# Kernel optimization log

Hardware: AMD Instinct MI355X
Metric: run time of the kernel (lower is better)

The kernel has to match this reference:

```python
import jax, jax.numpy as jnp
import numpy as np

N_NODES = 100_000
N_EDGES = 800_000
N_RELS = 2
NEG_SLOPE = 0.2  # DGL GATConv default negative_slope


def _gat_conv(x, src, dst, W, al, ar, b, n_nodes):
    """One DGL-style GATConv over one relation's edge list.
    x: (N, F_in); src/dst: (E,); W: (F_in, H*D); al/ar: (H, D); b: (H*D,).
    Returns (N, H, D). Zero in-degree nodes get just the bias (softmax empty)."""
    H, D = al.shape
    feat = (x @ W).reshape(-1, H, D)                      # (N, H, D)
    el = jnp.sum(feat * al, axis=-1)                      # (N, H)
    er = jnp.sum(feat * ar, axis=-1)                      # (N, H)
    e = jax.nn.leaky_relu(el[src] + er[dst], NEG_SLOPE)   # (E, H) edge scores
    # segment softmax over incoming edges of each dst node
    m = jax.ops.segment_max(e, dst, num_segments=n_nodes)  # (N, H)
    m = jax.lax.stop_gradient(jnp.where(jnp.isfinite(m), m, 0.0))
    ex = jnp.exp(e - m[dst])                              # (E, H)
    s = jax.ops.segment_sum(ex, dst, num_segments=n_nodes)  # (N, H)
    alpha = ex / s[dst]                                   # (E, H); s[dst] > 0 on edges
    # weighted scatter-aggregate of source features
    out = jax.ops.segment_sum(alpha[:, :, None] * feat[src], dst,
                              num_segments=n_nodes)       # (N, H, D)
    return out + b.reshape(H, D)


def reference(x, W1, al1, ar1, b1, W2, al2, ar2, b2, src, dst):
    n = x.shape[0]
    n_rels = src.shape[0]
    # layer 1: per-relation GATConv (2 heads), mean across relations
    h1 = sum(_gat_conv(x, src[r], dst[r], W1[r], al1[r], ar1[r], b1[r], n)
             for r in range(n_rels)) / n_rels             # (N, 2, 64)
    h1 = jax.nn.relu(h1.reshape(n, -1))                   # flatten(1) + relu -> (N, 128)
    # layer 2: per-relation GATConv (1 head), mean across relations, squeeze head
    h2 = sum(_gat_conv(h1, src[r], dst[r], W2[r], al2[r], ar2[r], b2[r], n)
             for r in range(n_rels)) / n_rels             # (N, 1, 128)
    return h2[:, 0, :]                                    # (N, 128)


def setup_inputs() -> dict:
    key = jax.random.key(0)
    ks = jax.random.split(key, 11)
    f = lambda k, s: jax.random.normal(k, s, dtype=jnp.float32) * 0.1
    return {
        "x": jax.random.normal(ks[0], (N_NODES, 128), dtype=jnp.float32),
        "W1": f(ks[1], (N_RELS, 128, 128)),
        "al1": f(ks[2], (N_RELS, 2, 64)),
        "ar1": f(ks[3], (N_RELS, 2, 64)),
        "b1": jnp.zeros((N_RELS, 128), jnp.float32),
        "W2": f(ks[4], (N_RELS, 128, 128)),
        "al2": f(ks[5], (N_RELS, 1, 128)),
        "ar2": f(ks[6], (N_RELS, 1, 128)),
        "b2": jnp.zeros((N_RELS, 128), jnp.float32),
        "src": jax.random.randint(ks[7], (N_RELS, N_EDGES), 0, N_NODES, dtype=jnp.int32),
        "dst": jax.random.randint(ks[8], (N_RELS, N_EDGES), 0, N_NODES, dtype=jnp.int32),
    }
```

## Files before the change

### kernel.cpp

```cpp
#include <hip/hip_runtime.h>
#include <hip/hip_bf16.h>
#include <math.h>

#define NN 100000
#define NE 800000
#define FD 128

#define BKW 512
#define NBK 391
#define CAP 4608
#define CHUNK 8192

typedef unsigned short ushort_t;
typedef __attribute__((ext_vector_type(8))) short bf16x8;
typedef __attribute__((ext_vector_type(4))) float f32x4;

union U8 { uint4 u; bf16x8 b; };

__device__ inline unsigned f2bf(float f){
    unsigned u = __float_as_uint(f);
    return (u + 0x7fffu + ((u >> 16) & 1u)) >> 16;
}
__device__ inline unsigned cvtpk(float lo, float hi){
    unsigned r;
    asm("v_cvt_pk_bf16_f32 %0, %1, %2" : "=v"(r) : "v"(lo), "v"(hi));
    return r;
}
__device__ inline float blo(unsigned p){ return __uint_as_float(p << 16); }
__device__ inline float bhi(unsigned p){ return __uint_as_float(p & 0xffff0000u); }
__device__ inline float2 up2(unsigned p){ float2 f; f.x = blo(p); f.y = bhi(p); return f; }
__device__ inline void pkfma(float2& d, float2 a, float2 b){
    asm("v_pk_fma_f32 %0, %1, %2, %0" : "+v"(d) : "v"(a), "v"(b));
}

__global__ __launch_bounds__(256) void k_part(const int* __restrict__ dst,
                                              const int* __restrict__ src,
                                              int* __restrict__ bcur,
                                              uint2* __restrict__ ebuf){
    __shared__ int lcount[NBK];
    __shared__ int lbase[NBK];
    int t = threadIdx.x;
    long base = (long)blockIdx.x * CHUNK;
    for (int j = t; j < NBK; j += 256) lcount[j] = 0;
    __syncthreads();
    #pragma unroll 4
    for (int k = 0; k < CHUNK/256; k++){
        long i = base + k*256 + t;
        if (i < 2*NE){
            int b = (dst[i] + ((i >= NE) ? NN : 0)) >> 9;
            atomicAdd(&lcount[b], 1);
        }
    }
    __syncthreads();
    for (int j = t; j < NBK; j += 256){
        int c = lcount[j];
        lbase[j] = c ? atomicAdd(&bcur[j], c) : 0;
    }
    __syncthreads();
    for (int j = t; j < NBK; j += 256) lcount[j] = 0;
    __syncthreads();
    #pragma unroll 4
    for (int k = 0; k < CHUNK/256; k++){
        long i = base + k*256 + t;
        if (i < 2*NE){
            int dstU = dst[i] + ((i >= NE) ? NN : 0);
            int b = dstU >> 9;
            int r = atomicAdd(&lcount[b], 1);
            int pos = lbase[b] + r;
            if (pos < (b + 1) * CAP)
                ebuf[pos] = make_uint2((unsigned)src[i], (unsigned)dstU);
        }
    }
}

__global__ __launch_bounds__(512) void k_bktscan(const int* __restrict__ bcur,
                                                 int* __restrict__ gbase,
                                                 int* __restrict__ rowptr){
    __shared__ int sm[512];
    int t = threadIdx.x;
    int v = (t < NBK) ? min(bcur[t] - t*CAP, CAP) : 0;
    sm[t] = v; __syncthreads();
    for (int off = 1; off < 512; off <<= 1){
        int add = (t >= off) ? sm[t-off] : 0;
        __syncthreads();
        sm[t] += add;
        __syncthreads();
    }
    if (t <= NBK) gbase[t] = sm[t] - v;
    if (t == 0) rowptr[2*NN] = 2*NE;
}

__global__ __launch_bounds__(256) void k_bscatter(const uint2* __restrict__ ebuf,
                                                  const int* __restrict__ bcur,
                                                  const int* __restrict__ gbase,
                                                  int* __restrict__ rowptr,
                                                  int* __restrict__ colsrc){
    __shared__ uint2 se[CAP];
    __shared__ int lhist[BKW];
    __shared__ int lcur[BKW];
    __shared__ int sm[256];
    int b = blockIdx.x;
    int n0 = b * BKW;
    int nloc = min(2*NN, n0 + BKW) - n0;
    int ecnt = min(bcur[b] - b*CAP, CAP);
    const uint2* eb = ebuf + (size_t)b * CAP;
    int t = threadIdx.x;
    lhist[2*t] = 0; lhist[2*t+1] = 0;
    __syncthreads();
    for (int i = t; i < ecnt; i += 256){
        uint2 e = eb[i];
        se[i] = e;
        atomicAdd(&lhist[e.y - n0], 1);
    }
    __syncthreads();
    int a0 = lhist[2*t], a1 = lhist[2*t+1];
    int ps = a0 + a1;
    sm[t] = ps; __syncthreads();
    for (int off = 1; off < 256; off <<= 1){
        int add = (t >= off) ? sm[t-off] : 0;
        __syncthreads();
        sm[t] += add;
        __syncthreads();
    }
    int excl = sm[t] - ps;
    int g = gbase[b];
    int p0 = g + excl, p1 = g + excl + a0;
    if (2*t     < nloc) rowptr[n0 + 2*t]     = p0;
    if (2*t + 1 < nloc) rowptr[n0 + 2*t + 1] = p1;
    lcur[2*t] = p0; lcur[2*t+1] = p1;
    __syncthreads();
    for (int i = t; i < ecnt; i += 256){
        uint2 e = se[i];
        int p = atomicAdd(&lcur[e.y - n0], 1);
        colsrc[p] = (int)e.x;
    }
}

__global__ void k_prepw2(const float* __restrict__ W1, const float* __restrict__ W2,
                         ushort_t* __restrict__ Wt1, ushort_t* __restrict__ Wt2,
                         int* __restrict__ bcur){
    int idx = blockIdx.x * blockDim.x + threadIdx.x;
    if (idx >= 65536){
        int t = idx - 65536;
        if (t < NBK) bcur[t] = t * CAP;
        return;
    }
    int m = idx >> 15;
    int i = idx & 32767;
    const float* W = m ? W2 : W1;
    ushort_t* Wt   = m ? Wt2 : Wt1;
    int j  = i & 7;
    int l  = (i >> 3) & 63;
    int ks = (i >> 9) & 3;
    int f  = i >> 11;
    int k  = ks*32 + (l >> 4)*8 + j;
    if (m) k = (((k & 7) >> 1) + 4*(k & 1))*16 + (k >> 3);
    int col = (f & 7)*16 + (l & 15);
    int rel = f >> 3;
    Wt[i] = (ushort_t)f2bf(W[rel*16384 + k*FD + col]);
}

__device__ inline float red16(float v){
    v += __shfl_xor(v, 1);
    v += __shfl_xor(v, 2);
    v += __shfl_xor(v, 4);
    v += __shfl_xor(v, 8);
    return v;
}

template<int H, bool AF32>
__global__ __launch_bounds__(256) void k_gemm_mfma(
        const ushort_t* __restrict__ Ab, const float* __restrict__ Af,
        const ushort_t* __restrict__ Wt,
        const float* __restrict__ al0, const float* __restrict__ ar0,
        const float* __restrict__ al1, const float* __restrict__ ar1,
        ushort_t* __restrict__ featb0, ushort_t* __restrict__ featb1,
        float* __restrict__ el0, float* __restrict__ er0,
        float* __restrict__ el1, float* __restrict__ er1){
    int t = threadIdx.x;
    int w = t >> 6, l = t & 63;
    int c = l & 15, kgrp = l >> 4;
    const bf16x8* WtV = (const bf16x8*)Wt;
    long arow = (long)blockIdx.x*64 + w*16 + c;
    bf16x8 zero8 = {0,0,0,0,0,0,0,0};
    bf16x8 af[4];
    bool rok = arow < NN;
    if (AF32){
        const float4* xv = (const float4*)Af;
        #pragma unroll
        for (int ks = 0; ks < 4; ks++){
            if (rok){
                float4 u = xv[arow*32 + (ks*4 + kgrp)*2];
                float4 v = xv[arow*32 + (ks*4 + kgrp)*2 + 1];
                U8 q;
                q.u = make_uint4(cvtpk(u.x,u.y), cvtpk(u.z,u.w),
                                 cvtpk(v.x,v.y), cvtpk(v.z,v.w));
                af[ks] = q.b;
            } else af[ks] = zero8;
        }
    } else {
        const bf16x8* AbV = (const bf16x8*)Ab;
        #pragma unroll
        for (int ks = 0; ks < 4; ks++)
            af[ks] = rok ? AbV[arow*16 + ks*4 + kgrp] : zero8;
    }
    f32x4 acc[16];
    #pragma unroll
    for (int f = 0; f < 16; f++) acc[f] = (f32x4){0.f,0.f,0.f,0.f};
    #pragma unroll
    for (int f = 0; f < 16; f++){
        #pragma unroll
        for (int ks = 0; ks < 4; ks++){
            acc[f] = __builtin_amdgcn_mfma_f32_16x16x32_bf16(
                         af[ks], WtV[(f*4 + ks)*64 + l], acc[f], 0, 0, 0);
        }
    }
    float alv0[8], arv0[8], alv1[8], arv1[8];
    #pragma unroll
    for (int f = 0; f < 8; f++){
        alv0[f] = al0[f*16 + c]; arv0[f] = ar0[f*16 + c];
        alv1[f] = al1[f*16 + c]; arv1[f] = ar1[f*16 + c];
    }
    #pragma unroll
    for (int reg = 0; reg < 4; reg++){
        long orow = (long)blockIdx.x*64 + w*16 + kgrp*4 + reg;
        bool ok = orow < NN;
        if (ok){
            uint4 p0, p1;
            p0.x = cvtpk(acc[0][reg],  acc[4][reg]);
            p0.y = cvtpk(acc[1][reg],  acc[5][reg]);
            p0.z = cvtpk(acc[2][reg],  acc[6][reg]);
            p0.w = cvtpk(acc[3][reg],  acc[7][reg]);
            p1.x = cvtpk(acc[8][reg],  acc[12][reg]);
            p1.y = cvtpk(acc[9][reg],  acc[13][reg]);
            p1.z = cvtpk(acc[10][reg], acc[14][reg]);
            p1.w = cvtpk(acc[11][reg], acc[15][reg]);
            *(uint4*)&featb0[orow*FD + c*8] = p0;
            *(uint4*)&featb1[orow*FD + c*8] = p1;
        }
        if (H == 2){
            float pl00=0, pr00=0, pl01=0, pr01=0;
            float pl10=0, pr10=0, pl11=0, pr11=0;
            #pragma unroll
            for (int f = 0; f < 4; f++){
                pl00 = fmaf(acc[f][reg],    alv0[f],   pl00);
                pr00 = fmaf(acc[f][reg],    arv0[f],   pr00);
                pl01 = fmaf(acc[4+f][reg],  alv0[4+f], pl01);
                pr01 = fmaf(acc[4+f][reg],  arv0[4+f], pr01);
                pl10 = fmaf(acc[8+f][reg],  alv1[f],   pl10);
                pr10 = fmaf(acc[8+f][reg],  arv1[f],   pr10);
                pl11 = fmaf(acc[12+f][reg], alv1[4+f], pl11);
                pr11 = fmaf(acc[12+f][reg], arv1[4+f], pr11);
            }
            pl00 = red16(pl00); pr00 = red16(pr00);
            pl01 = red16(pl01); pr01 = red16(pr01);
            pl10 = red16(pl10); pr10 = red16(pr10);
            pl11 = red16(pl11); pr11 = red16(pr11);
            if (c == 0 && ok){
                el0[orow*2] = pl00; el0[orow*2+1] = pl01;
                er0[orow*2] = pr00; er0[orow*2+1] = pr01;
                el1[orow*2] = pl10; el1[orow*2+1] = pl11;
                er1[orow*2] = pr10; er1[orow*2+1] = pr11;
            }
        } else {
            float pl0=0, pr0=0, pl1=0, pr1=0;
            #pragma unroll
            for (int f = 0; f < 8; f++){
                pl0 = fmaf(acc[f][reg],   alv0[f], pl0);
                pr0 = fmaf(acc[f][reg],   arv0[f], pr0);
                pl1 = fmaf(acc[8+f][reg], alv1[f], pl1);
                pr1 = fmaf(acc[8+f][reg], arv1[f], pr1);
            }
            pl0 = red16(pl0); pr0 = red16(pr0);
            pl1 = red16(pl1); pr1 = red16(pr1);
            if (c == 0 && ok){
                el0[orow] = pl0; er0[orow] = pr0;
                el1[orow] = pl1; er1[orow] = pr1;
            }
        }
    }
}

template<int H>
__global__ __launch_bounds__(256) void k_agg2(
                       const int* __restrict__ rowptr,
                       const int* __restrict__ colsrc,
                       const float* __restrict__ el0, const float* __restrict__ er0,
                       const float* __restrict__ el1, const float* __restrict__ er1,
                       const ushort_t* __restrict__ featb0, const ushort_t* __restrict__ featb1,
                       const float* __restrict__ bias0, const float* __restrict__ bias1,
                       ushort_t* __restrict__ outb, float* __restrict__ outf){
    __shared__ float4 stg[4][2][2][32];
    int wid  = threadIdx.x >> 6;
    int lane = threadIdx.x & 63;
    int half = lane >> 5;
    int hl   = lane & 31;
    int sub  = lane & 15;
    int g    = (lane >> 4) & 1;
    int node = ((blockIdx.x * blockDim.x + threadIdx.x) >> 6) * 2 + half;
    if (node >= NN) return;
    int base0 = rowptr[node],       end0 = rowptr[node+1];
    int base1 = rowptr[NN + node],  end1 = rowptr[NN + node + 1];
    bool has0 = end0 > base0, has1 = end1 > base1;
    float er00 = er0[node*H];
    float er01 = (H == 2) ? er0[node*H + 1] : 0.f;
    float er10 = er1[node*H];
    float er11 = (H == 2) ? er1[node*H + 1] : 0.f;
    float2 ap0[4], ap1[4];
    #pragma unroll
    for (int i = 0; i < 4; i++){ ap0[i] = make_float2(0.f,0.f); ap1[i] = make_float2(0.f,0.f); }
    float s00=0.f, s01=0.f, s10=0.f, s11=0.f;
    while (base0 < end0 || base1 < end1){
        int nrem0 = end0 - base0, nrem1 = end1 - base1;
        bool act0 = hl < nrem0, act1 = hl < nrem1;
        int sv0 = act0 ? colsrc[base0 + hl] : 0;
        int sv1 = act1 ? colsrc[base1 + hl] : 0;
        float a00=0.f, a01=0.f, a10=0.f, a11=0.f;
        if (act0){
            if (H == 2){
                float2 e2 = *(const float2*)&el0[sv0*2];
                float e0 = e2.x + er00, e1 = e2.y + er01;
                e0 = (e0 > 0.f) ? e0 : 0.2f*e0;
                e1 = (e1 > 0.f) ? e1 : 0.2f*e1;
                a00 = __expf(e0); a01 = __expf(e1);
            } else {
                float e0 = el0[sv0] + er00;
                e0 = (e0 > 0.f) ? e0 : 0.2f*e0;
                a00 = __expf(e0);
            }
        }
        if (act1){
            if (H == 2){
                float2 e2 = *(const float2*)&el1[sv1*2];
                float e0 = e2.x + er10, e1 = e2.y + er11;
                e0 = (e0 > 0.f) ? e0 : 0.2f*e0;
                e1 = (e1 > 0.f) ? e1 : 0.2f*e1;
                a10 = __expf(e0); a11 = __expf(e1);
            } else {
                float e0 = el1[sv1] + er10;
                e0 = (e0 > 0.f) ? e0 : 0.2f*e0;
                a10 = __expf(e0);
            }
        }
        s00 += a00; s01 += a01; s10 += a10; s11 += a11;
        stg[wid][half][0][hl] = make_float4(__int_as_float(sv0), a00,
                                            (H == 2) ? a01 : a00, 0.f);
        stg[wid][half][1][hl] = make_float4(__int_as_float(sv1), a10,
                                            (H == 2) ? a11 : a10, 0.f);
        __builtin_amdgcn_sched_barrier(0);
        int nn0 = (nrem0 > 0) ? min(32, nrem0) : 0;
        int nn1 = (nrem1 > 0) ? min(32, nrem1) : 0;
        int nnm = (nn0 > nn1) ? nn0 : nn1;
        for (int j4 = 0; j4 < nnm; j4 += 4){
            int sA = j4 + g, sB = sA + 2;
            float4 e0A = stg[wid][half][0][sA];
            float4 e0B = stg[wid][half][0][sB];
            float4 e1A = stg[wid][half][1][sA];
            float4 e1B = stg[wid][half][1][sB];
            uint4 p0A = *(const uint4*)&featb0[__float_as_uint(e0A.x)*FD + sub*8];
            uint4 p0B = *(const uint4*)&featb0[__float_as_uint(e0B.x)*FD + sub*8];
            uint4 p1A = *(const uint4*)&featb1[__float_as_uint(e1A.x)*FD + sub*8];
            uint4 p1B = *(const uint4*)&featb1[__float_as_uint(e1B.x)*FD + sub*8];
            float2 w0A = make_float2(e0A.y, e0A.z);
            float2 w0B = make_float2(e0B.y, e0B.z);
            float2 w1A = make_float2(e1A.y, e1A.z);
            float2 w1B = make_float2(e1B.y, e1B.z);
            pkfma(ap0[0], w0A, up2(p0A.x));
            pkfma(ap0[1], w0A, up2(p0A.y));
            pkfma(ap0[2], w0A, up2(p0A.z));
            pkfma(ap0[3], w0A, up2(p0A.w));
            pkfma(ap0[0], w0B, up2(p0B.x));
            pkfma(ap0[1], w0B, up2(p0B.y));
            pkfma(ap0[2], w0B, up2(p0B.z));
            pkfma(ap0[3], w0B, up2(p0B.w));
            pkfma(ap1[0], w1A, up2(p1A.x));
            pkfma(ap1[1], w1A, up2(p1A.y));
            pkfma(ap1[2], w1A, up2(p1A.z));
            pkfma(ap1[3], w1A, up2(p1A.w));
            pkfma(ap1[0], w1B, up2(p1B.x));
            pkfma(ap1[1], w1B, up2(p1B.y));
            pkfma(ap1[2], w1B, up2(p1B.z));
            pkfma(ap1[3], w1B, up2(p1B.w));
        }
        base0 += 32; base1 += 32;
    }
    #pragma unroll
    for (int off = 16; off > 0; off >>= 1){
        s00 += __shfl_xor(s00, off);
        s10 += __shfl_xor(s10, off);
        if (H == 2){ s01 += __shfl_xor(s01, off); s11 += __shfl_xor(s11, off); }
    }
    #pragma unroll
    for (int i = 0; i < 4; i++){
        ap0[i].x += __shfl_xor(ap0[i].x, 16); ap0[i].y += __shfl_xor(ap0[i].y, 16);
        ap1[i].x += __shfl_xor(ap1[i].x, 16); ap1[i].y += __shfl_xor(ap1[i].y, 16);
    }
    if (hl < 16){
        float i00 = has0 ? 1.f/s00 : 0.f;
        float i01 = (H == 2) ? (has0 ? 1.f/s01 : 0.f) : i00;
        float i10 = has1 ? 1.f/s10 : 0.f;
        float i11 = (H == 2) ? (has1 ? 1.f/s11 : 0.f) : i10;
        float2 vp[4];
        #pragma unroll
        for (int t = 0; t < 4; t++){
            float bx = bias0[t*16 + sub]       + bias1[t*16 + sub];
            float by = bias0[(t+4)*16 + sub]   + bias1[(t+4)*16 + sub];
            vp[t].x = 0.5f*(ap0[t].x*i00 + ap1[t].x*i10 + bx);
            vp[t].y = 0.5f*(ap0[t].y*i01 + ap1[t].y*i11 + by);
        }
        if (H == 2){
            #pragma unroll
            for (int t = 0; t < 4; t++){
                vp[t].x = fmaxf(vp[t].x, 0.f);
                vp[t].y = fmaxf(vp[t].y, 0.f);
            }
            uint4 o;
            o.x = cvtpk(vp[0].x, vp[0].y); o.y = cvtpk(vp[1].x, vp[1].y);
            o.z = cvtpk(vp[2].x, vp[2].y); o.w = cvtpk(vp[3].x, vp[3].y);
            *(uint4*)&outb[(size_t)node*FD + sub*8] = o;
        } else {
            #pragma unroll
            for (int t = 0; t < 4; t++){
                outf[(size_t)node*FD + t*16 + sub]     = vp[t].x;
                outf[(size_t)node*FD + (t+4)*16 + sub] = vp[t].y;
            }
        }
    }
}

extern "C" void kernel_launch(void* const* d_in, const int* in_sizes, int n_in,
                              void* d_out, int out_size, void* d_ws, size_t ws_size,
                              hipStream_t stream){
    const float* x   = (const float*)d_in[0];
    const float* W1  = (const float*)d_in[1];
    const float* al1 = (const float*)d_in[2];
    const float* ar1 = (const float*)d_in[3];
    const float* b1  = (const float*)d_in[4];
    const float* W2  = (const float*)d_in[5];
    const float* al2 = (const float*)d_in[6];
    const float* ar2 = (const float*)d_in[7];
    const float* b2  = (const float*)d_in[8];
    const int*   src = (const int*)d_in[9];
    const int*   dst = (const int*)d_in[10];
    float* out = (float*)d_out;

    size_t off = 0;
    auto carve = [&](size_t bytes) -> char* {
        char* p = (char*)d_ws + off;
        off += (bytes + 255) & ~(size_t)255;
        return p;
    };
    ushort_t* h1b    = (ushort_t*)carve((size_t)NN * FD * 2);
    ushort_t* featb0 = (ushort_t*)carve((size_t)NN * FD * 2);
    ushort_t* featb1 = (ushort_t*)carve((size_t)NN * FD * 2);
    ushort_t* Wt1    = (ushort_t*)carve(32768 * 2);
    ushort_t* Wt2    = (ushort_t*)carve(32768 * 2);
    float* el0      = (float*)carve((size_t)NN * 2 * 4);
    float* er0      = (float*)carve((size_t)NN * 2 * 4);
    float* el1      = (float*)carve((size_t)NN * 2 * 4);
    float* er1      = (float*)carve((size_t)NN * 2 * 4);
    int*   rowptrA  = (int*)  carve((size_t)(2*NN + 1) * 4);
    int*   colsrcA  = (int*)  carve((size_t)2*NE * 4);
    int*   bcur     = (int*)  carve((size_t)NBK * 4);
    int*   gbase    = (int*)  carve((size_t)(NBK + 1) * 4);
    if (off > ws_size) return;
    uint2* ebuf = (uint2*)featb0;

    const int PB = (2*NE + CHUNK - 1) / CHUNK;
    const int GB = (NN + 63) / 64;
    const int WB = (NN + 7) / 8;
    const int PWB = (65536 + NBK + 255) / 256;

    k_prepw2<<<PWB, 256, 0, stream>>>(W1, W2, Wt1, Wt2, bcur);

    k_part<<<PB, 256, 0, stream>>>(dst, src, bcur, ebuf);
    k_bktscan<<<1, 512, 0, stream>>>(bcur, gbase, rowptrA);
    k_bscatter<<<NBK, 256, 0, stream>>>(ebuf, bcur, gbase, rowptrA, colsrcA);

    k_gemm_mfma<2, true><<<GB, 256, 0, stream>>>(nullptr, x, Wt1,
                                           al1, ar1, al1 + FD, ar1 + FD,
                                           featb0, featb1, el0, er0, el1, er1);
    k_agg2<2><<<WB, 256, 0, stream>>>(rowptrA, colsrcA,
                                      el0, er0, el1, er1, featb0, featb1,
                                      b1, b1 + FD, h1b, nullptr);

    k_gemm_mfma<1, false><<<GB, 256, 0, stream>>>(h1b, nullptr, Wt2,
                                           al2, ar2, al2 + FD, ar2 + FD,
                                           featb0, featb1, el0, er0, el1, er1);
    k_agg2<1><<<WB, 256, 0, stream>>>(rowptrA, colsrcA,
                                      el0, er0, el1, er1, featb0, featb1,
                                      b2, b2 + FD, nullptr, out);
}
```

Measured before the change: 283.9 us.

## Merge CSR build and layer-1 GEMM into fewer launches with atomic bucket bases

Packs the edge partition and the weight conversion into one launch, and the bucket scatter and the first-layer GEMM into a second launch, so independent work runs side by side. The global bucket scan kernel is removed. Each bucket block now claims its output base with an atomic counter, and rows are described by separate begin/end arrays instead of a single rowptr. ebuf gets its own workspace buffer so it no longer aliases featb0, which the concurrent GEMM writes. Buckets are laid out out of order in colsrc, and a memset launch is added to reset the counters.

After: 260.8 us. 8.1% less time.

```diff
diff --git a/kernel.cpp b/kernel.cpp
--- a/kernel.cpp
+++ b/kernel.cpp
@@ -10,6 +10,8 @@
 #define NBK 391
 #define CAP 4608
 #define CHUNK 8192
+#define PB   196
+#define GB   1563
 
 typedef unsigned short ushort_t;
 typedef __attribute__((ext_vector_type(8))) short bf16x8;
@@ -33,10 +35,9 @@
     asm("v_pk_fma_f32 %0, %1, %2, %0" : "+v"(d) : "v"(a), "v"(b));
 }
 
-__global__ __launch_bounds__(256) void k_part(const int* __restrict__ dst,
-                                              const int* __restrict__ src,
-                                              int* __restrict__ bcur,
-                                              uint2* __restrict__ ebuf){
+
+__device__ void part_body(const int* __restrict__ dst, const int* __restrict__ src,
+                          int* __restrict__ bcur, uint2* __restrict__ ebuf){
     __shared__ int lcount[NBK];
     __shared__ int lbase[NBK];
     int t = threadIdx.x;
@@ -67,84 +68,15 @@
             int b = dstU >> 9;
             int r = atomicAdd(&lcount[b], 1);
             int pos = lbase[b] + r;
-            if (pos < (b + 1) * CAP)
-                ebuf[pos] = make_uint2((unsigned)src[i], (unsigned)dstU);
-        }
-    }
-}
-
-__global__ __launch_bounds__(512) void k_bktscan(const int* __restrict__ bcur,
-                                                 int* __restrict__ gbase,
-                                                 int* __restrict__ rowptr){
-    __shared__ int sm[512];
-    int t = threadIdx.x;
-    int v = (t < NBK) ? min(bcur[t] - t*CAP, CAP) : 0;
-    sm[t] = v; __syncthreads();
-    for (int off = 1; off < 512; off <<= 1){
-        int add = (t >= off) ? sm[t-off] : 0;
-        __syncthreads();
-        sm[t] += add;
-        __syncthreads();
-    }
-    if (t <= NBK) gbase[t] = sm[t] - v;
-    if (t == 0) rowptr[2*NN] = 2*NE;
-}
-
-__global__ __launch_bounds__(256) void k_bscatter(const uint2* __restrict__ ebuf,
-                                                  const int* __restrict__ bcur,
-                                                  const int* __restrict__ gbase,
-                                                  int* __restrict__ rowptr,
-                                                  int* __restrict__ colsrc){
-    __shared__ uint2 se[CAP];
-    __shared__ int lhist[BKW];
-    __shared__ int lcur[BKW];
-    __shared__ int sm[256];
-    int b = blockIdx.x;
-    int n0 = b * BKW;
-    int nloc = min(2*NN, n0 + BKW) - n0;
-    int ecnt = min(bcur[b] - b*CAP, CAP);
-    const uint2* eb = ebuf + (size_t)b * CAP;
-    int t = threadIdx.x;
-    lhist[2*t] = 0; lhist[2*t+1] = 0;
-    __syncthreads();
-    for (int i = t; i < ecnt; i += 256){
-        uint2 e = eb[i];
-        se[i] = e;
-        atomicAdd(&lhist[e.y - n0], 1);
-    }
-    __syncthreads();
-    int a0 = lhist[2*t], a1 = lhist[2*t+1];
-    int ps = a0 + a1;
-    sm[t] = ps; __syncthreads();
-    for (int off = 1; off < 256; off <<= 1){
-        int add = (t >= off) ? sm[t-off] : 0;
-        __syncthreads();
-        sm[t] += add;
-        __syncthreads();
-    }
-    int excl = sm[t] - ps;
-    int g = gbase[b];
-    int p0 = g + excl, p1 = g + excl + a0;
-    if (2*t     < nloc) rowptr[n0 + 2*t]     = p0;
-    if (2*t + 1 < nloc) rowptr[n0 + 2*t + 1] = p1;
-    lcur[2*t] = p0; lcur[2*t+1] = p1;
-    __syncthreads();
-    for (int i = t; i < ecnt; i += 256){
-        uint2 e = se[i];
-        int p = atomicAdd(&lcur[e.y - n0], 1);
-        colsrc[p] = (int)e.x;
-    }
-}
-
-__global__ void k_prepw2(const float* __restrict__ W1, const float* __restrict__ W2,
-                         ushort_t* __restrict__ Wt1, ushort_t* __restrict__ Wt2,
-                         int* __restrict__ bcur){
-    int idx = blockIdx.x * blockDim.x + threadIdx.x;
-    if (idx >= 65536){
-        int t = idx - 65536;
-        if (t < NBK) bcur[t] = t * CAP;
-        return;
-    }
+            if (pos < CAP)
+                ebuf[(size_t)b*CAP + pos] = make_uint2((unsigned)src[i], (unsigned)dstU);
+        }
+    }
+}
+
+__device__ void prepw_body(int idx, const float* __restrict__ W1,
+                           const float* __restrict__ W2,
+                           ushort_t* __restrict__ Wt1, ushort_t* __restrict__ Wt2){
     int m = idx >> 15;
     int i = idx & 32767;
     const float* W = m ? W2 : W1;
@@ -160,6 +92,48 @@
     Wt[i] = (ushort_t)f2bf(W[rel*16384 + k*FD + col]);
 }
 
+__device__ void bscatter_body(int b, const uint2* __restrict__ ebuf,
+                              const int* __restrict__ bcur, int* __restrict__ gcounter,
+                              int* __restrict__ rowbeg, int* __restrict__ rowend,
+                              int* __restrict__ colsrc){
+    __shared__ int lhist[BKW];
+    __shared__ int lcur[BKW];
+    __shared__ int sm[256];
+    __shared__ int gb;
+    int n0 = b * BKW;
+    int nloc = min(2*NN, n0 + BKW) - n0;
+    int ecnt = min(bcur[b], CAP);
+    const uint2* eb = ebuf + (size_t)b * CAP;
+    int t = threadIdx.x;
+    lhist[2*t] = 0; lhist[2*t+1] = 0;
+    __syncthreads();
+    for (int i = t; i < ecnt; i += 256)
+        atomicAdd(&lhist[eb[i].y - n0], 1);
+    __syncthreads();
+    int a0 = lhist[2*t], a1 = lhist[2*t+1];
+    int ps = a0 + a1;
+    sm[t] = ps; __syncthreads();
+    for (int off = 1; off < 256; off <<= 1){
+        int add = (t >= off) ? sm[t-off] : 0;
+        __syncthreads();
+        sm[t] += add;
+        __syncthreads();
+    }
+    if (t == 255) gb = atomicAdd(gcounter, sm[255]);
+    __syncthreads();
+    int excl = sm[t] - ps;
+    int p0 = gb + excl, p1 = gb + excl + a0;
+    if (2*t < nloc){ rowbeg[n0 + 2*t] = p0; rowend[n0 + 2*t] = p0 + a0; }
+    if (2*t + 1 < nloc){ rowbeg[n0 + 2*t + 1] = p1; rowend[n0 + 2*t + 1] = p1 + a1; }
+    lcur[2*t] = p0; lcur[2*t+1] = p1;
+    __syncthreads();
+    for (int i = t; i < ecnt; i += 256){
+        uint2 e = eb[i];
+        int p = atomicAdd(&lcur[e.y - n0], 1);
+        colsrc[p] = (int)e.x;
+    }
+}
+
 __device__ inline float red16(float v){
     v += __shfl_xor(v, 1);
     v += __shfl_xor(v, 2);
@@ -169,7 +143,7 @@
 }
 
 template<int H, bool AF32>
-__global__ __launch_bounds__(256) void k_gemm_mfma(
+__device__ void gemm_body(int bid,
         const ushort_t* __restrict__ Ab, const float* __restrict__ Af,
         const ushort_t* __restrict__ Wt,
         const float* __restrict__ al0, const float* __restrict__ ar0,
@@ -181,7 +155,7 @@
     int w = t >> 6, l = t & 63;
     int c = l & 15, kgrp = l >> 4;
     const bf16x8* WtV = (const bf16x8*)Wt;
-    long arow = (long)blockIdx.x*64 + w*16 + c;
+    long arow = (long)bid*64 + w*16 + c;
     bf16x8 zero8 = {0,0,0,0,0,0,0,0};
     bf16x8 af[4];
     bool rok = arow < NN;
@@ -223,7 +197,7 @@
     }
     #pragma unroll
     for (int reg = 0; reg < 4; reg++){
-        long orow = (long)blockIdx.x*64 + w*16 + kgrp*4 + reg;
+        long orow = (long)bid*64 + w*16 + kgrp*4 + reg;
         bool ok = orow < NN;
         if (ok){
             uint4 p0, p1;
@@ -281,9 +255,55 @@
     }
 }
 
+__global__ __launch_bounds__(256) void kA(const int* __restrict__ dst,
+                                          const int* __restrict__ src,
+                                          int* __restrict__ bcur,
+                                          uint2* __restrict__ ebuf,
+                                          const float* __restrict__ W1,
+                                          const float* __restrict__ W2,
+                                          ushort_t* __restrict__ Wt1,
+                                          ushort_t* __restrict__ Wt2){
+    if (blockIdx.x < PB){
+        part_body(dst, src, bcur, ebuf);
+        return;
+    }
+    int idx = (blockIdx.x - PB) * 256 + threadIdx.x;
+    prepw_body(idx, W1, W2, Wt1, Wt2);
+}
+
+__global__ __launch_bounds__(256) void kB(
+        const uint2* __restrict__ ebuf, const int* __restrict__ bcur,
+        int* __restrict__ gcounter, int* __restrict__ rowbeg,
+        int* __restrict__ rowend, int* __restrict__ colsrc,
+        const float* __restrict__ Af, const ushort_t* __restrict__ Wt,
+        const float* __restrict__ al0, const float* __restrict__ ar0,
+        const float* __restrict__ al1, const float* __restrict__ ar1,
+        ushort_t* __restrict__ featb0, ushort_t* __restrict__ featb1,
+        float* __restrict__ el0, float* __restrict__ er0,
+        float* __restrict__ el1, float* __restrict__ er1){
+    if (blockIdx.x < NBK){
+        bscatter_body(blockIdx.x, ebuf, bcur, gcounter, rowbeg, rowend, colsrc);
+        return;
+    }
+    gemm_body<2, true>(blockIdx.x - NBK, nullptr, Af, Wt, al0, ar0, al1, ar1,
+                       featb0, featb1, el0, er0, el1, er1);
+}
+
+__global__ __launch_bounds__(256) void k_gemm2(
+        const ushort_t* __restrict__ Ab, const ushort_t* __restrict__ Wt,
+        const float* __restrict__ al0, const float* __restrict__ ar0,
+        const float* __restrict__ al1, const float* __restrict__ ar1,
+        ushort_t* __restrict__ featb0, ushort_t* __restrict__ featb1,
+        float* __restrict__ el0, float* __restrict__ er0,
+        float* __restrict__ el1, float* __restrict__ er1){
+    gemm_body<1, false>(blockIdx.x, Ab, nullptr, Wt, al0, ar0, al1, ar1,
+                        featb0, featb1, el0, er0, el1, er1);
+}
+
 template<int H>
 __global__ __launch_bounds__(256) void k_agg2(
-                       const int* __restrict__ rowptr,
+                       const int* __restrict__ rowbeg,
+                       const int* __restrict__ rowend,
                        const int* __restrict__ colsrc,
                        const float* __restrict__ el0, const float* __restrict__ er0,
                        const float* __restrict__ el1, const float* __restrict__ er1,
@@ -299,8 +319,8 @@
     int g    = (lane >> 4) & 1;
     int node = ((blockIdx.x * blockDim.x + threadIdx.x) >> 6) * 2 + half;
     if (node >= NN) return;
-    int base0 = rowptr[node],       end0 = rowptr[node+1];
-    int base1 = rowptr[NN + node],  end1 = rowptr[NN + node + 1];
+    int base0 = rowbeg[node],       end0 = rowend[node];
+    int base1 = rowbeg[NN + node],  end1 = rowend[NN + node];
     bool has0 = end0 > base0, has1 = end1 > base1;
     float er00 = er0[node*H];
     float er01 = (H == 2) ? er0[node*H + 1] : 0.f;
@@ -453,41 +473,37 @@
     ushort_t* h1b    = (ushort_t*)carve((size_t)NN * FD * 2);
     ushort_t* featb0 = (ushort_t*)carve((size_t)NN * FD * 2);
     ushort_t* featb1 = (ushort_t*)carve((size_t)NN * FD * 2);
+    uint2*    ebuf   = (uint2*)   carve((size_t)NBK * CAP * 8);
     ushort_t* Wt1    = (ushort_t*)carve(32768 * 2);
     ushort_t* Wt2    = (ushort_t*)carve(32768 * 2);
     float* el0      = (float*)carve((size_t)NN * 2 * 4);
     float* er0      = (float*)carve((size_t)NN * 2 * 4);
     float* el1      = (float*)carve((size_t)NN * 2 * 4);
     float* er1      = (float*)carve((size_t)NN * 2 * 4);
-    int*   rowptrA  = (int*)  carve((size_t)(2*NN + 1) * 4);
+    int*   rowbeg   = (int*)  carve((size_t)2*NN * 4);
+    int*   rowend   = (int*)  carve((size_t)2*NN * 4);
     int*   colsrcA  = (int*)  carve((size_t)2*NE * 4);
-    int*   bcur     = (int*)  carve((size_t)NBK * 4);
-    int*   gbase    = (int*)  carve((size_t)(NBK + 1) * 4);
+    int*   bcur     = (int*)  carve((size_t)(NBK + 1) * 4);
     if (off > ws_size) return;
-    uint2* ebuf = (uint2*)featb0;
-
-    const int PB = (2*NE + CHUNK - 1) / CHUNK;
-    const int GB = (NN + 63) / 64;
+    int* gcounter = bcur + NBK;
+
     const int WB = (NN + 7) / 8;
-    const int PWB = (65536 + NBK + 255) / 256;
-
-    k_prepw2<<<PWB, 256, 0, stream>>>(W1, W2, Wt1, Wt2, bcur);
-
-    k_part<<<PB, 256, 0, stream>>>(dst, src, bcur, ebuf);
-    k_bktscan<<<1, 512, 0, stream>>>(bcur, gbase, rowptrA);
-    k_bscatter<<<NBK, 256, 0, stream>>>(ebuf, bcur, gbase, rowptrA, colsrcA);
-
-    k_gemm_mfma<2, true><<<GB, 256, 0, stream>>>(nullptr, x, Wt1,
-                                           al1, ar1, al1 + FD, ar1 + FD,
-                                           featb0, featb1, el0, er0, el1, er1);
-    k_agg2<2><<<WB, 256, 0, stream>>>(rowptrA, colsrcA,
+
+    hipMemsetAsync(bcur, 0, (size_t)(NBK + 1) * 4, stream);
+
+    kA<<<PB + 256, 256, 0, stream>>>(dst, src, bcur, ebuf, W1, W2, Wt1, Wt2);
+
+    kB<<<NBK + GB, 256, 0, stream>>>(ebuf, bcur, gcounter, rowbeg, rowend, colsrcA,
+                                     x, Wt1, al1, ar1, al1 + FD, ar1 + FD,
+                                     featb0, featb1, el0, er0, el1, er1);
+
+    k_agg2<2><<<WB, 256, 0, stream>>>(rowbeg, rowend, colsrcA,
                                       el0, er0, el1, er1, featb0, featb1,
                                       b1, b1 + FD, h1b, nullptr);
 
-    k_gemm_mfma<1, false><<<GB, 256, 0, stream>>>(h1b, nullptr, Wt2,
-                                           al2, ar2, al2 + FD, ar2 + FD,
-                                           featb0, featb1, el0, er0, el1, er1);
-    k_agg2<1><<<WB, 256, 0, stream>>>(rowptrA, colsrcA,
+    k_gemm2<<<GB, 256, 0, stream>>>(h1b, Wt2, al2, ar2, al2 + FD, ar2 + FD,
+                                    featb0, featb1, el0, er0, el1, er1);
+    k_agg2<1><<<WB, 256, 0, stream>>>(rowbeg, rowend, colsrcA,
                                       el0, er0, el1, er1, featb0, featb1,
                                       b2, b2 + FD, nullptr, out);
 }
```
